# Performance work log

Measured on AMD Instinct MI355X. Metric: run time of the kernel, lower is better.

Reference implementation:

```python
import jax, jax.numpy as jnp
import numpy as np

# dims: episodes E, steps S, comm length L, hidden H, rnn input IN, comm vocab OUT
E, S, L, H, IN, OUT = 64, 32, 32, 1024, 2048, 64
TAU = 2.0      # MTRNN leaky-integrator time constant
EPS = 1e-5     # BatchNorm eps


def setup_inputs() -> dict:
    key = jax.random.key(0)
    ks = jax.random.split(key, 16)
    def p(k, shape, scale=0.02):
        return jax.random.normal(k, shape, jnp.float32) * scale
    return {
        "h_w_action": jax.random.normal(ks[0], (E, S, IN), jnp.float32),
        # MTRNN cell
        "Wx": p(ks[1], (IN, H)), "bx": jnp.zeros((H,), jnp.float32),
        "Wh": p(ks[2], (H, H)), "bh": jnp.zeros((H,), jnp.float32),
        # Ted_Conv1d: 4 branches, kernels 1/3/5/7, each H//4 out channels (OIH layout)
        "w1": p(ks[3], (H // 4, H, 1)), "b1": jnp.zeros((H // 4,), jnp.float32),
        "w3": p(ks[4], (H // 4, H, 3)), "b3": jnp.zeros((H // 4,), jnp.float32),
        "w5": p(ks[5], (H // 4, H, 5)), "b5": jnp.zeros((H // 4,), jnp.float32),
        "w7": p(ks[6], (H // 4, H, 7)), "b7": jnp.zeros((H // 4,), jnp.float32),
        # BatchNorm1d affine
        "gamma": jnp.ones((H,), jnp.float32), "beta": jnp.zeros((H,), jnp.float32),
        # PReLU (single shared slope, torch default init 0.25)
        "prelu_a": jnp.array(0.25, jnp.float32),
        # output Linear
        "Wout": p(ks[7], (H, OUT)), "bout": jnp.zeros((OUT,), jnp.float32),
    }


def _conv(x, w, b):
    # x: [N, C, L], w: [O, I, k], 'same' padding for odd kernels
    pad = (w.shape[-1] - 1) // 2
    y = jax.lax.conv_general_dilated(x, w, (1,), [(pad, pad)],
                                     dimension_numbers=('NCH', 'OIH', 'NCH'))
    return y + b[None, :, None]


def reference(h_w_action, Wx, bx, Wh, bh, w1, b1, w3, b3, w5, b5, w7, b7,
              gamma, beta, prelu_a, Wout, bout):
    # MTRNN: same input every step; leaky integration h' = (1-1/tau)h + (1/tau)tanh(Wx x + Wh h)
    x_r = h_w_action @ Wx + bx                      # [E,S,H], constant across steps
    h0 = jnp.zeros((E, S, H), h_w_action.dtype)

    def step(h, _):
        h_new = (1.0 - 1.0 / TAU) * h + (1.0 / TAU) * jnp.tanh(x_r + h @ Wh + bh)
        return h_new, h_new

    _, hs = jax.lax.scan(step, h0, None, length=L)  # [L,E,S,H]
    hs = hs.transpose(1, 2, 0, 3).reshape(E * S, L, H)

    # multi-kernel conv over the comm-length axis
    xc = hs.transpose(0, 2, 1)                      # [N,H,L]
    y = jnp.concatenate([_conv(xc, w1, b1), _conv(xc, w3, b3),
                         _conv(xc, w5, b5), _conv(xc, w7, b7)], axis=1)  # [N,H,L]

    # BatchNorm1d (training-mode batch stats over N and L), affine
    mean = y.mean(axis=(0, 2), keepdims=True)
    var = y.var(axis=(0, 2), keepdims=True)
    y = (y - mean) * jax.lax.rsqrt(var + EPS) * gamma[None, :, None] + beta[None, :, None]

    # PReLU; Dropout is identity at eval
    y = jnp.where(y > 0, y, prelu_a * y)

    y = y.transpose(0, 2, 1).reshape(E, S, L, H)
    return y @ Wout + bout                          # [E,S,L,OUT]
```

## Files before the change

kernel.cpp:

```cpp
#include <hip/hip_runtime.h>
#include <cstdint>
#include <cmath>

#define DI __device__ __forceinline__


typedef __attribute__((ext_vector_type(8))) short bf16x8;
typedef __attribute__((ext_vector_type(4))) short s16x4;
typedef __attribute__((ext_vector_type(4))) float f32x4;

DI float bf2f(short u){
  union { unsigned int i; float f; } v; v.i = ((unsigned int)(unsigned short)u) << 16; return v.f;
}
DI short f2bf(float f){
  unsigned int x = __builtin_bit_cast(unsigned int, f);
  unsigned int r = (x + 0x7FFFu + ((x >> 16) & 1u)) >> 16;
  return (short)(unsigned short)r;
}
DI void gload16(const void* g, void* l){
  __builtin_amdgcn_global_load_lds(
      (const __attribute__((address_space(1))) unsigned int*)g,
      (__attribute__((address_space(3))) unsigned int*)l, 16, 0, 0);
}

template<int BM, int BN, int MODE>
__global__ __launch_bounds__(256)
void gemm_k(const short* __restrict__ A, long lda,
            const short* __restrict__ Bt, long ldb, int Ksteps,
            const float* __restrict__ bias,
            float* __restrict__ f32out,
            const float* __restrict__ f32in,
            short* __restrict__ bfout, int jj)
{
  constexpr int WTM = BM / 2, WTN = BN / 2;
  constexpr int FM = WTM / 16, FN = WTN / 16;
  constexpr int AIT = BM / 32, BIT = BN / 32;
  __shared__ short As[BM * 64];
  __shared__ short Bs[BN * 64];
  const int tid = threadIdx.x;
  const int w = tid >> 6, l = tid & 63;
  const int wr = w >> 1, wc = w & 1;
  const int lr = l & 15, lk = (l >> 4) << 3;
  const int brow = blockIdx.x * BM;
  const int bcol = blockIdx.y * BN;

  int coff = 0, jout = 0;
  if constexpr (MODE == 2) {
    const int bb = bcol >> 7;
    const int dlt = (bb < 2) ? -3 : (bb < 6) ? -2 : (bb < 12) ? -1
                  : (bb < 20) ? 0 : (bb < 26) ? 1 : (bb < 30) ? 2 : 3;
    coff = (dlt == -3) ? 768 : (dlt == -2) ? 256 : (dlt == -1) ? -512
         : (dlt == 0) ? -1536 : (dlt == 1) ? -2304 : (dlt == 2) ? -2816 : -3072;
    jout = jj - dlt;
    if (jout < 0 || jout > 31) return;
  }

  f32x4 acc[FM][FN];
  #pragma unroll
  for (int i = 0; i < FM; i++)
    #pragma unroll
    for (int j = 0; j < FN; j++) {
      acc[i][j][0] = 0.f; acc[i][j][1] = 0.f; acc[i][j][2] = 0.f; acc[i][j][3] = 0.f;
    }

  const short* ap[AIT];
  const short* bp[BIT];
  const int rsub = tid >> 3;
  const int koff = (tid & 7) << 3;
  #pragma unroll
  for (int it = 0; it < AIT; ++it)
    ap[it] = A + (long)(brow + it * 32 + rsub) * lda + koff;
  #pragma unroll
  for (int it = 0; it < BIT; ++it)
    bp[it] = Bt + (long)(bcol + it * 32 + rsub) * ldb + koff;

  for (int ks = 0; ks < Ksteps; ++ks) {
    #pragma unroll
    for (int it = 0; it < AIT; ++it) {
      gload16(ap[it], As + ((it * 256 + (w << 6)) << 3));
      ap[it] += 64;
    }
    #pragma unroll
    for (int it = 0; it < BIT; ++it) {
      gload16(bp[it], Bs + ((it * 256 + (w << 6)) << 3));
      bp[it] += 64;
    }
    __syncthreads();
    #pragma unroll
    for (int kk = 0; kk < 64; kk += 32) {
      bf16x8 a[FM], b[FN];
      #pragma unroll
      for (int i = 0; i < FM; i++)
        a[i] = *(const bf16x8*)&As[(wr * WTM + i * 16 + lr) * 64 + kk + lk];
      #pragma unroll
      for (int j = 0; j < FN; j++)
        b[j] = *(const bf16x8*)&Bs[(wc * WTN + j * 16 + lr) * 64 + kk + lk];
      #pragma unroll
      for (int i = 0; i < FM; i++)
        #pragma unroll
        for (int j = 0; j < FN; j++)
          acc[i][j] = __builtin_amdgcn_mfma_f32_16x16x32_bf16(a[i], b[j], acc[i][j], 0, 0, 0);
    }
    __syncthreads();
  }

  const int rbase = brow + wr * WTM;
  const int cbase = bcol + wc * WTN;
  const int rl = (l >> 4) << 2;
  #pragma unroll
  for (int i = 0; i < FM; i++) {
    #pragma unroll
    for (int j = 0; j < FN; j++) {
      #pragma unroll
      for (int r = 0; r < 4; r++) {
        const int row = rbase + i * 16 + rl + r;
        const int col = cbase + j * 16 + lr;
        const float v = acc[i][j][r];
        if constexpr (MODE == 0) {
          f32out[(long)row * 1024 + col] = v + bias[col];
        } else if constexpr (MODE == 1) {
          const long idx = (long)row * 1024 + col;
          const float hn = 0.5f * f32out[idx] + 0.5f * tanhf(f32in[idx] + v + bias[col]);
          f32out[idx] = hn;
          bfout[idx] = f2bf(hn);
        } else if constexpr (MODE == 2) {
          short* yp = bfout + ((long)row * 32 + jout) * 1024 + (col + coff);
          *yp = f2bf(bf2f(*yp) + v);
        } else {
          f32out[(long)row * 64 + col] = v + bias[col];
        }
      }
    }
  }
}

__global__ __launch_bounds__(256)
void g5_bn(const short* __restrict__ y, const short* __restrict__ WoutT,
           const float* __restrict__ scal, const float* __restrict__ shft,
           const float* __restrict__ aP, const float* __restrict__ bout,
           float* __restrict__ out)
{
  __shared__ short As[128 * 64];
  __shared__ short Bs[64 * 64];
  __shared__ float sS[1024], sB[1024];
  const int tid = threadIdx.x;
  const int w = tid >> 6, l = tid & 63;
  const int wr = w >> 1, wc = w & 1;
  const int lr = l & 15, lk = (l >> 4) << 3;
  const int m0 = blockIdx.x * 128;
  for (int i = tid; i < 1024; i += 256) { sS[i] = scal[i]; sB[i] = shft[i]; }
  const float a = *aP;
  __syncthreads();

  f32x4 acc[4][2];
  #pragma unroll
  for (int i = 0; i < 4; i++)
    #pragma unroll
    for (int j = 0; j < 2; j++) {
      acc[i][j][0] = 0.f; acc[i][j][1] = 0.f; acc[i][j][2] = 0.f; acc[i][j][3] = 0.f;
    }

  const int rsub = tid >> 3;
  const int koff = (tid & 7) << 3;
  const short* yp[4];
  #pragma unroll
  for (int it = 0; it < 4; ++it)
    yp[it] = y + (long)(m0 + it * 32 + rsub) * 1024 + koff;
  const short* bp[2];
  #pragma unroll
  for (int it = 0; it < 2; ++it)
    bp[it] = WoutT + (long)(it * 32 + rsub) * 1024 + koff;

  for (int ks = 0; ks < 16; ++ks) {
    #pragma unroll
    for (int it = 0; it < 2; ++it) {
      gload16(bp[it], Bs + ((it * 256 + (w << 6)) << 3));
      bp[it] += 64;
    }
    const int c0 = ks * 64 + koff;
    #pragma unroll
    for (int it = 0; it < 4; ++it) {
      bf16x8 v = *(const bf16x8*)yp[it];
      yp[it] += 64;
      #pragma unroll
      for (int e = 0; e < 8; ++e) {
        float f = bf2f(v[e]) * sS[c0 + e] + sB[c0 + e];
        v[e] = f2bf(f > 0.f ? f : a * f);
      }
      *(bf16x8*)(As + ((it * 256 + tid) << 3)) = v;
    }
    __syncthreads();
    #pragma unroll
    for (int kk = 0; kk < 64; kk += 32) {
      bf16x8 af[4], bf_[2];
      #pragma unroll
      for (int i = 0; i < 4; i++)
        af[i] = *(const bf16x8*)&As[(wr * 64 + i * 16 + lr) * 64 + kk + lk];
      #pragma unroll
      for (int j = 0; j < 2; j++)
        bf_[j] = *(const bf16x8*)&Bs[(wc * 32 + j * 16 + lr) * 64 + kk + lk];
      #pragma unroll
      for (int i = 0; i < 4; i++)
        #pragma unroll
        for (int j = 0; j < 2; j++)
          acc[i][j] = __builtin_amdgcn_mfma_f32_16x16x32_bf16(af[i], bf_[j], acc[i][j], 0, 0, 0);
    }
    __syncthreads();
  }

  const int rbase = m0 + wr * 64, cbase = wc * 32;
  const int rl = (l >> 4) << 2;
  #pragma unroll
  for (int i = 0; i < 4; i++)
    #pragma unroll
    for (int j = 0; j < 2; j++)
      #pragma unroll
      for (int r = 0; r < 4; r++) {
        const int row = rbase + i * 16 + rl + r;
        const int col = cbase + j * 16 + lr;
        out[(long)row * 64 + col] = acc[i][j][r] + bout[col];
      }
}

__global__ void zero16(float4* __restrict__ p, long n)
{
  long i = (long)blockIdx.x * 256 + threadIdx.x;
  if (i < n) p[i] = float4{0.f, 0.f, 0.f, 0.f};
}

__global__ void cvt4_f32_bf16(const float* __restrict__ in, short* __restrict__ out, int n4)
{
  int i = blockIdx.x * 256 + threadIdx.x;
  if (i >= n4) return;
  float4 v = ((const float4*)in)[i];
  s16x4 o; o[0] = f2bf(v.x); o[1] = f2bf(v.y); o[2] = f2bf(v.z); o[3] = f2bf(v.w);
  ((s16x4*)out)[i] = o;
}

__global__ void transpose_f32_bf16(const float* __restrict__ in, short* __restrict__ out,
                                   int R, int C)
{
  __shared__ short tile[32][33];
  const int tx = threadIdx.x & 31, ty = threadIdx.x >> 5;
  const int c0 = blockIdx.x * 32, r0 = blockIdx.y * 32;
  #pragma unroll
  for (int i = 0; i < 32; i += 8)
    tile[ty + i][tx] = f2bf(in[(long)(r0 + ty + i) * C + (c0 + tx)]);
  __syncthreads();
  #pragma unroll
  for (int i = 0; i < 32; i += 8)
    out[(long)(c0 + ty + i) * R + (r0 + tx)] = tile[tx][ty + i];
}

__global__ void build_wpack(const float* __restrict__ w1, const float* __restrict__ w3,
                            const float* __restrict__ w5, const float* __restrict__ w7,
                            short* __restrict__ Wp)
{
  const int pc = blockIdx.x;
  int dlt, c;
  if      (pc < 256)  { dlt = -3; c = pc + 768; }
  else if (pc < 768)  { dlt = -2; c = pc + 256; }
  else if (pc < 1536) { dlt = -1; c = pc - 512; }
  else if (pc < 2560) { dlt = 0;  c = pc - 1536; }
  else if (pc < 3328) { dlt = 1;  c = pc - 2304; }
  else if (pc < 3840) { dlt = 2;  c = pc - 2816; }
  else                { dlt = 3;  c = pc - 3072; }
  const int b = c >> 8, kb = 2 * b + 1, t = dlt + b, oo = c & 255;
  const float* w = (b == 0) ? w1 : (b == 1) ? w3 : (b == 2) ? w5 : w7;
  short* dst = Wp + (long)pc * 1024;
  for (int i = threadIdx.x; i < 1024; i += 256)
    dst[i] = f2bf(w[((long)oo * 1024 + i) * kb + t]);
}

__global__ void bn_stats(const short* __restrict__ y, float* __restrict__ sum,
                         float* __restrict__ ssq)
{
  const int c0 = threadIdx.x * 4;
  float s0 = 0, s1 = 0, s2 = 0, s3 = 0, q0 = 0, q1 = 0, q2 = 0, q3 = 0;
  const long base = (long)blockIdx.x * 32;
  for (int r = 0; r < 32; ++r) {
    s16x4 v = *(const s16x4*)(y + (base + r) * 1024 + c0);
    float f0 = bf2f(v[0]), f1 = bf2f(v[1]), f2v = bf2f(v[2]), f3 = bf2f(v[3]);
    s0 += f0; s1 += f1; s2 += f2v; s3 += f3;
    q0 += f0 * f0; q1 += f1 * f1; q2 += f2v * f2v; q3 += f3 * f3;
  }
  atomicAdd(&sum[c0 + 0], s0); atomicAdd(&sum[c0 + 1], s1);
  atomicAdd(&sum[c0 + 2], s2); atomicAdd(&sum[c0 + 3], s3);
  atomicAdd(&ssq[c0 + 0], q0); atomicAdd(&ssq[c0 + 1], q1);
  atomicAdd(&ssq[c0 + 2], q2); atomicAdd(&ssq[c0 + 3], q3);
}

__global__ void bn_finalize(const float* __restrict__ bnsum, const float* __restrict__ bnss,
                            const float* __restrict__ gamma, const float* __restrict__ beta,
                            float* __restrict__ scale, float* __restrict__ shift)
{
  int c = blockIdx.x * 256 + threadIdx.x;
  const float inv = 1.f / 65536.f;
  float mean = bnsum[c] * inv;
  float var = bnss[c] * inv - mean * mean;
  float sc = gamma[c] * rsqrtf(var + 1e-5f);
  scale[c] = sc;
  shift[c] = beta[c] - mean * sc;
}

extern "C" void kernel_launch(void* const* d_in, const int* in_sizes, int n_in,
                              void* d_out, int out_size, void* d_ws, size_t ws_size,
                              hipStream_t stream)
{
  const float* h_w_action = (const float*)d_in[0];
  const float* Wx   = (const float*)d_in[1];
  const float* bx   = (const float*)d_in[2];
  const float* Wh   = (const float*)d_in[3];
  const float* bh   = (const float*)d_in[4];
  const float* w1   = (const float*)d_in[5];
  const float* w3   = (const float*)d_in[7];
  const float* w5   = (const float*)d_in[9];
  const float* w7   = (const float*)d_in[11];
  const float* gamma = (const float*)d_in[13];
  const float* beta  = (const float*)d_in[14];
  const float* prelu = (const float*)d_in[15];
  const float* Wout  = (const float*)d_in[16];
  const float* bout  = (const float*)d_in[17];
  float* out = (float*)d_out;

  char* p = (char*)d_ws;
  auto alloc = [&](size_t bytes) -> char* {
    char* r = p; p += (bytes + 255) & ~(size_t)255; return r;
  };
  short* y     = (short*)alloc(65536L * 1024 * 2);
  float* xr    = (float*)alloc(2048L * 1024 * 4);
  float* hf    = (float*)alloc(2048L * 1024 * 4);
  short* hb0   = (short*)alloc(2048L * 1024 * 2);
  short* hb1   = (short*)alloc(2048L * 1024 * 2);
  short* A1    = (short*)alloc(2048L * 2048 * 2);
  short* WxT   = (short*)alloc(1024L * 2048 * 2);
  short* WhT   = (short*)alloc(1024L * 1024 * 2);
  short* Wp    = (short*)alloc(4096L * 1024 * 2);
  short* WoutT = (short*)alloc(64L * 1024 * 2);
  float* bnsum = (float*)alloc(1024 * 4);
  float* bnss  = (float*)alloc(1024 * 4);
  float* scal  = (float*)alloc(1024 * 4);
  float* shft  = (float*)alloc(1024 * 4);

  if ((size_t)(p - (char*)d_ws) > ws_size) return;

  zero16<<<32768, 256, 0, stream>>>((float4*)y, 65536L * 1024 * 2 / 16);
  zero16<<<2048, 256, 0, stream>>>((float4*)hf, 2048L * 1024 * 4 / 16);
  zero16<<<1024, 256, 0, stream>>>((float4*)hb0, 2048L * 1024 * 2 / 16);
  zero16<<<1, 256, 0, stream>>>((float4*)bnsum, 256);
  zero16<<<1, 256, 0, stream>>>((float4*)bnss, 256);

  cvt4_f32_bf16<<<4096, 256, 0, stream>>>(h_w_action, A1, 2048 * 2048 / 4);
  transpose_f32_bf16<<<dim3(32, 64), 256, 0, stream>>>(Wx, WxT, 2048, 1024);
  transpose_f32_bf16<<<dim3(32, 32), 256, 0, stream>>>(Wh, WhT, 1024, 1024);
  transpose_f32_bf16<<<dim3(2, 32), 256, 0, stream>>>(Wout, WoutT, 1024, 64);
  build_wpack<<<4096, 256, 0, stream>>>(w1, w3, w5, w7, Wp);

  gemm_k<64, 128, 0><<<dim3(32, 8), 256, 0, stream>>>(
      A1, 2048, WxT, 2048, 32, bx, xr, nullptr, nullptr, 0);

  short* hb[2] = {hb0, hb1};
  for (int s = 1; s <= 32; ++s) {
    gemm_k<64, 64, 1><<<dim3(32, 16), 256, 0, stream>>>(
        hb[(s - 1) & 1], 1024, WhT, 1024, 16, bh, hf, xr, hb[s & 1], 0);
    gemm_k<128, 128, 2><<<dim3(16, 32), 256, 0, stream>>>(
        hb[s & 1], 1024, Wp, 1024, 16, nullptr, nullptr, nullptr, y, s - 1);
  }

  bn_stats<<<2048, 256, 0, stream>>>(y, bnsum, bnss);
  bn_finalize<<<4, 256, 0, stream>>>(bnsum, bnss, gamma, beta, scal, shft);

  g5_bn<<<dim3(512, 1), 256, 0, stream>>>(y, WoutT, scal, shft, prelu, bout, out);
}
```

Baseline: 2.044 ms.

## Double-buffer GEMM LDS loads, drop y/hf zeroing, replace BN atomics with two-pass reduction

The GEMM main loop now double-buffers its LDS tiles so the next K-tile's global-to-LDS loads overlap the current MFMA compute, using explicit vmcnt waits and raw barriers. The recurrent step reads the previous hidden state from the bf16 buffer instead of a separate fp32 copy. That removes the fp32 hidden state and its zeroing, but the leaky integration now runs at bf16 precision. The conv accumulation writes directly on the first contributing tap, so the large y buffer no longer needs zeroing. BN statistics use per-block partial sums plus a second reduction kernel instead of atomics, and the xr GEMM tile shrinks to 64x64.

```diff
diff --git a/kernel.cpp b/kernel.cpp
--- a/kernel.cpp
+++ b/kernel.cpp
@@ -21,6 +21,12 @@
   __builtin_amdgcn_global_load_lds(
       (const __attribute__((address_space(1))) unsigned int*)g,
       (__attribute__((address_space(3))) unsigned int*)l, 16, 0, 0);
+}
+template<int N> DI void waitv(){
+  if constexpr (N == 0) asm volatile("s_waitcnt vmcnt(0)" ::: "memory");
+  else if constexpr (N == 4) asm volatile("s_waitcnt vmcnt(4)" ::: "memory");
+  else if constexpr (N == 6) asm volatile("s_waitcnt vmcnt(6)" ::: "memory");
+  else asm volatile("s_waitcnt vmcnt(8)" ::: "memory");
 }
 
 template<int BM, int BN, int MODE>
@@ -35,8 +41,9 @@
   constexpr int WTM = BM / 2, WTN = BN / 2;
   constexpr int FM = WTM / 16, FN = WTN / 16;
   constexpr int AIT = BM / 32, BIT = BN / 32;
-  __shared__ short As[BM * 64];
-  __shared__ short Bs[BN * 64];
+  constexpr int NLD = AIT + BIT;
+  __shared__ short As[2][BM * 64];
+  __shared__ short Bs[2][BN * 64];
   const int tid = threadIdx.x;
   const int w = tid >> 6, l = tid & 63;
   const int wr = w >> 1, wc = w & 1;
@@ -45,6 +52,7 @@
   const int bcol = blockIdx.y * BN;
 
   int coff = 0, jout = 0;
+  bool first = false;
   if constexpr (MODE == 2) {
     const int bb = bcol >> 7;
     const int dlt = (bb < 2) ? -3 : (bb < 6) ? -2 : (bb < 12) ? -1
@@ -53,6 +61,8 @@
          : (dlt == 0) ? -1536 : (dlt == 1) ? -2304 : (dlt == 2) ? -2816 : -3072;
     jout = jj - dlt;
     if (jout < 0 || jout > 31) return;
+    const int ubranch = (bcol + coff) >> 8;
+    first = (dlt == -(ubranch < jout ? ubranch : jout));
   }
 
   f32x4 acc[FM][FN];
@@ -63,45 +73,54 @@
       acc[i][j][0] = 0.f; acc[i][j][1] = 0.f; acc[i][j][2] = 0.f; acc[i][j][3] = 0.f;
     }
 
-  const short* ap[AIT];
-  const short* bp[BIT];
   const int rsub = tid >> 3;
   const int koff = (tid & 7) << 3;
+  const short* aB[AIT];
+  const short* bB[BIT];
   #pragma unroll
   for (int it = 0; it < AIT; ++it)
-    ap[it] = A + (long)(brow + it * 32 + rsub) * lda + koff;
+    aB[it] = A + (long)(brow + it * 32 + rsub) * lda + koff;
   #pragma unroll
   for (int it = 0; it < BIT; ++it)
-    bp[it] = Bt + (long)(bcol + it * 32 + rsub) * ldb + koff;
-
-  for (int ks = 0; ks < Ksteps; ++ks) {
-    #pragma unroll
-    for (int it = 0; it < AIT; ++it) {
-      gload16(ap[it], As + ((it * 256 + (w << 6)) << 3));
-      ap[it] += 64;
-    }
-    #pragma unroll
-    for (int it = 0; it < BIT; ++it) {
-      gload16(bp[it], Bs + ((it * 256 + (w << 6)) << 3));
-      bp[it] += 64;
-    }
-    __syncthreads();
+    bB[it] = Bt + (long)(bcol + it * 32 + rsub) * ldb + koff;
+
+  auto stage = [&](int ks, int bsel) {
+    const int off = ks * 64;
+    #pragma unroll
+    for (int it = 0; it < AIT; ++it)
+      gload16(aB[it] + off, &As[bsel][(it * 256 + (w << 6)) << 3]);
+    #pragma unroll
+    for (int it = 0; it < BIT; ++it)
+      gload16(bB[it] + off, &Bs[bsel][(it * 256 + (w << 6)) << 3]);
+  };
+  auto compute = [&](int bsel) {
     #pragma unroll
     for (int kk = 0; kk < 64; kk += 32) {
       bf16x8 a[FM], b[FN];
       #pragma unroll
       for (int i = 0; i < FM; i++)
-        a[i] = *(const bf16x8*)&As[(wr * WTM + i * 16 + lr) * 64 + kk + lk];
+        a[i] = *(const bf16x8*)&As[bsel][(wr * WTM + i * 16 + lr) * 64 + kk + lk];
       #pragma unroll
       for (int j = 0; j < FN; j++)
-        b[j] = *(const bf16x8*)&Bs[(wc * WTN + j * 16 + lr) * 64 + kk + lk];
+        b[j] = *(const bf16x8*)&Bs[bsel][(wc * WTN + j * 16 + lr) * 64 + kk + lk];
       #pragma unroll
       for (int i = 0; i < FM; i++)
         #pragma unroll
         for (int j = 0; j < FN; j++)
           acc[i][j] = __builtin_amdgcn_mfma_f32_16x16x32_bf16(a[i], b[j], acc[i][j], 0, 0, 0);
     }
-    __syncthreads();
+  };
+
+  stage(0, 0);
+  for (int t = 0; t < Ksteps; ++t) {
+    const int cur = t & 1;
+    if (t + 1 < Ksteps) { stage(t + 1, cur ^ 1); waitv<NLD>(); }
+    else                { waitv<0>(); }
+    __builtin_amdgcn_s_barrier();
+    __builtin_amdgcn_sched_barrier(0);
+    compute(cur);
+    __builtin_amdgcn_sched_barrier(0);
+    __builtin_amdgcn_s_barrier();
   }
 
   const int rbase = brow + wr * WTM;
@@ -120,14 +139,13 @@
           f32out[(long)row * 1024 + col] = v + bias[col];
         } else if constexpr (MODE == 1) {
           const long idx = (long)row * 1024 + col;
-          const float hn = 0.5f * f32out[idx] + 0.5f * tanhf(f32in[idx] + v + bias[col]);
-          f32out[idx] = hn;
+          const float hp = bf2f(A[(long)row * lda + col]);
+          const float hn = 0.5f * hp + 0.5f * tanhf(f32in[idx] + v + bias[col]);
           bfout[idx] = f2bf(hn);
         } else if constexpr (MODE == 2) {
           short* yp = bfout + ((long)row * 32 + jout) * 1024 + (col + coff);
-          *yp = f2bf(bf2f(*yp) + v);
-        } else {
-          f32out[(long)row * 64 + col] = v + bias[col];
+          if (first) *yp = f2bf(v);
+          else       *yp = f2bf(bf2f(*yp) + v);
         }
       }
     }
@@ -272,32 +290,35 @@
     dst[i] = f2bf(w[((long)oo * 1024 + i) * kb + t]);
 }
 
-__global__ void bn_stats(const short* __restrict__ y, float* __restrict__ sum,
-                         float* __restrict__ ssq)
+__global__ void bn_stats1(const short* __restrict__ y, float* __restrict__ psum,
+                          float* __restrict__ pssq)
 {
   const int c0 = threadIdx.x * 4;
   float s0 = 0, s1 = 0, s2 = 0, s3 = 0, q0 = 0, q1 = 0, q2 = 0, q3 = 0;
-  const long base = (long)blockIdx.x * 32;
-  for (int r = 0; r < 32; ++r) {
+  const long base = (long)blockIdx.x * 64;
+  for (int r = 0; r < 64; ++r) {
     s16x4 v = *(const s16x4*)(y + (base + r) * 1024 + c0);
     float f0 = bf2f(v[0]), f1 = bf2f(v[1]), f2v = bf2f(v[2]), f3 = bf2f(v[3]);
     s0 += f0; s1 += f1; s2 += f2v; s3 += f3;
     q0 += f0 * f0; q1 += f1 * f1; q2 += f2v * f2v; q3 += f3 * f3;
   }
-  atomicAdd(&sum[c0 + 0], s0); atomicAdd(&sum[c0 + 1], s1);
-  atomicAdd(&sum[c0 + 2], s2); atomicAdd(&sum[c0 + 3], s3);
-  atomicAdd(&ssq[c0 + 0], q0); atomicAdd(&ssq[c0 + 1], q1);
-  atomicAdd(&ssq[c0 + 2], q2); atomicAdd(&ssq[c0 + 3], q3);
-}
-
-__global__ void bn_finalize(const float* __restrict__ bnsum, const float* __restrict__ bnss,
-                            const float* __restrict__ gamma, const float* __restrict__ beta,
-                            float* __restrict__ scale, float* __restrict__ shift)
-{
-  int c = blockIdx.x * 256 + threadIdx.x;
+  ((float4*)(psum + (long)blockIdx.x * 1024))[threadIdx.x] = float4{s0, s1, s2, s3};
+  ((float4*)(pssq + (long)blockIdx.x * 1024))[threadIdx.x] = float4{q0, q1, q2, q3};
+}
+
+__global__ void bn_stats2(const float* __restrict__ psum, const float* __restrict__ pssq,
+                          const float* __restrict__ gamma, const float* __restrict__ beta,
+                          float* __restrict__ scale, float* __restrict__ shift)
+{
+  const int c = blockIdx.x * 256 + threadIdx.x;
+  float s = 0.f, q = 0.f;
+  for (int b = 0; b < 1024; ++b) {
+    s += psum[(long)b * 1024 + c];
+    q += pssq[(long)b * 1024 + c];
+  }
   const float inv = 1.f / 65536.f;
-  float mean = bnsum[c] * inv;
-  float var = bnss[c] * inv - mean * mean;
+  float mean = s * inv;
+  float var = q * inv - mean * mean;
   float sc = gamma[c] * rsqrtf(var + 1e-5f);
   scale[c] = sc;
   shift[c] = beta[c] - mean * sc;
@@ -329,7 +350,8 @@
   };
   short* y     = (short*)alloc(65536L * 1024 * 2);
   float* xr    = (float*)alloc(2048L * 1024 * 4);
-  float* hf    = (float*)alloc(2048L * 1024 * 4);
+  float* psum  = (float*)alloc(1024L * 1024 * 4);
+  float* pssq  = (float*)alloc(1024L * 1024 * 4);
   short* hb0   = (short*)alloc(2048L * 1024 * 2);
   short* hb1   = (short*)alloc(2048L * 1024 * 2);
   short* A1    = (short*)alloc(2048L * 2048 * 2);
@@ -337,18 +359,12 @@
   short* WhT   = (short*)alloc(1024L * 1024 * 2);
   short* Wp    = (short*)alloc(4096L * 1024 * 2);
   short* WoutT = (short*)alloc(64L * 1024 * 2);
-  float* bnsum = (float*)alloc(1024 * 4);
-  float* bnss  = (float*)alloc(1024 * 4);
   float* scal  = (float*)alloc(1024 * 4);
   float* shft  = (float*)alloc(1024 * 4);
 
   if ((size_t)(p - (char*)d_ws) > ws_size) return;
 
-  zero16<<<32768, 256, 0, stream>>>((float4*)y, 65536L * 1024 * 2 / 16);
-  zero16<<<2048, 256, 0, stream>>>((float4*)hf, 2048L * 1024 * 4 / 16);
   zero16<<<1024, 256, 0, stream>>>((float4*)hb0, 2048L * 1024 * 2 / 16);
-  zero16<<<1, 256, 0, stream>>>((float4*)bnsum, 256);
-  zero16<<<1, 256, 0, stream>>>((float4*)bnss, 256);
 
   cvt4_f32_bf16<<<4096, 256, 0, stream>>>(h_w_action, A1, 2048 * 2048 / 4);
   transpose_f32_bf16<<<dim3(32, 64), 256, 0, stream>>>(Wx, WxT, 2048, 1024);
@@ -356,19 +372,19 @@
   transpose_f32_bf16<<<dim3(2, 32), 256, 0, stream>>>(Wout, WoutT, 1024, 64);
   build_wpack<<<4096, 256, 0, stream>>>(w1, w3, w5, w7, Wp);
 
-  gemm_k<64, 128, 0><<<dim3(32, 8), 256, 0, stream>>>(
+  gemm_k<64, 64, 0><<<dim3(32, 16), 256, 0, stream>>>(
       A1, 2048, WxT, 2048, 32, bx, xr, nullptr, nullptr, 0);
 
   short* hb[2] = {hb0, hb1};
   for (int s = 1; s <= 32; ++s) {
     gemm_k<64, 64, 1><<<dim3(32, 16), 256, 0, stream>>>(
-        hb[(s - 1) & 1], 1024, WhT, 1024, 16, bh, hf, xr, hb[s & 1], 0);
+        hb[(s - 1) & 1], 1024, WhT, 1024, 16, bh, nullptr, xr, hb[s & 1], 0);
     gemm_k<128, 128, 2><<<dim3(16, 32), 256, 0, stream>>>(
         hb[s & 1], 1024, Wp, 1024, 16, nullptr, nullptr, nullptr, y, s - 1);
   }
 
-  bn_stats<<<2048, 256, 0, stream>>>(y, bnsum, bnss);
-  bn_finalize<<<4, 256, 0, stream>>>(bnsum, bnss, gamma, beta, scal, shft);
+  bn_stats1<<<1024, 256, 0, stream>>>(y, psum, pssq);
+  bn_stats2<<<4, 256, 0, stream>>>(psum, pssq, gamma, beta, scal, shft);
 
   g5_bn<<<dim3(512, 1), 256, 0, stream>>>(y, WoutT, scal, shft, prelu, bout, out);
 }
```

Result: slower. 2.198 ms (+7.6%).

## Drop y zero-fill, fp32 hidden state, and atomic BN stats

Applied to the files above, without the earlier changes.

The conv GEMM now writes, rather than accumulates, on the first tap that touches each output slot, so the 128MB zero-fill of y goes away. The recurrence reads the previous hidden state from the bf16 A operand instead of keeping a separate fp32 state buffer, which removes that buffer's traffic and its zeroing. BatchNorm statistics move from atomics to per-block partial sums plus a second reduction kernel that also folds in the finalize step, and the x-projection GEMM tile is reduced. The risks are lower precision in the leaky-integrator state, since it is now carried in bf16, and correctness of the first-writer logic.

```diff
diff --git a/kernel.cpp b/kernel.cpp
--- a/kernel.cpp
+++ b/kernel.cpp
@@ -45,6 +45,7 @@
   const int bcol = blockIdx.y * BN;
 
   int coff = 0, jout = 0;
+  bool first = false;
   if constexpr (MODE == 2) {
     const int bb = bcol >> 7;
     const int dlt = (bb < 2) ? -3 : (bb < 6) ? -2 : (bb < 12) ? -1
@@ -53,6 +54,8 @@
          : (dlt == 0) ? -1536 : (dlt == 1) ? -2304 : (dlt == 2) ? -2816 : -3072;
     jout = jj - dlt;
     if (jout < 0 || jout > 31) return;
+    const int ubranch = (bcol + coff) >> 8;
+    first = (dlt == -(ubranch < jout ? ubranch : jout));
   }
 
   f32x4 acc[FM][FN];
@@ -63,10 +66,10 @@
       acc[i][j][0] = 0.f; acc[i][j][1] = 0.f; acc[i][j][2] = 0.f; acc[i][j][3] = 0.f;
     }
 
+  const int rsub = tid >> 3;
+  const int koff = (tid & 7) << 3;
   const short* ap[AIT];
   const short* bp[BIT];
-  const int rsub = tid >> 3;
-  const int koff = (tid & 7) << 3;
   #pragma unroll
   for (int it = 0; it < AIT; ++it)
     ap[it] = A + (long)(brow + it * 32 + rsub) * lda + koff;
@@ -120,14 +123,13 @@
           f32out[(long)row * 1024 + col] = v + bias[col];
         } else if constexpr (MODE == 1) {
           const long idx = (long)row * 1024 + col;
-          const float hn = 0.5f * f32out[idx] + 0.5f * tanhf(f32in[idx] + v + bias[col]);
-          f32out[idx] = hn;
+          const float hp = bf2f(A[(long)row * lda + col]);
+          const float hn = 0.5f * hp + 0.5f * tanhf(f32in[idx] + v + bias[col]);
           bfout[idx] = f2bf(hn);
         } else if constexpr (MODE == 2) {
           short* yp = bfout + ((long)row * 32 + jout) * 1024 + (col + coff);
-          *yp = f2bf(bf2f(*yp) + v);
-        } else {
-          f32out[(long)row * 64 + col] = v + bias[col];
+          if (first) *yp = f2bf(v);
+          else       *yp = f2bf(bf2f(*yp) + v);
         }
       }
     }
@@ -272,35 +274,57 @@
     dst[i] = f2bf(w[((long)oo * 1024 + i) * kb + t]);
 }
 
-__global__ void bn_stats(const short* __restrict__ y, float* __restrict__ sum,
-                         float* __restrict__ ssq)
+__global__ void bn_stats1(const short* __restrict__ y, float* __restrict__ psum,
+                          float* __restrict__ pssq)
 {
   const int c0 = threadIdx.x * 4;
   float s0 = 0, s1 = 0, s2 = 0, s3 = 0, q0 = 0, q1 = 0, q2 = 0, q3 = 0;
-  const long base = (long)blockIdx.x * 32;
-  for (int r = 0; r < 32; ++r) {
+  const long base = (long)blockIdx.x * 64;
+  for (int r = 0; r < 64; ++r) {
     s16x4 v = *(const s16x4*)(y + (base + r) * 1024 + c0);
     float f0 = bf2f(v[0]), f1 = bf2f(v[1]), f2v = bf2f(v[2]), f3 = bf2f(v[3]);
     s0 += f0; s1 += f1; s2 += f2v; s3 += f3;
     q0 += f0 * f0; q1 += f1 * f1; q2 += f2v * f2v; q3 += f3 * f3;
   }
-  atomicAdd(&sum[c0 + 0], s0); atomicAdd(&sum[c0 + 1], s1);
-  atomicAdd(&sum[c0 + 2], s2); atomicAdd(&sum[c0 + 3], s3);
-  atomicAdd(&ssq[c0 + 0], q0); atomicAdd(&ssq[c0 + 1], q1);
-  atomicAdd(&ssq[c0 + 2], q2); atomicAdd(&ssq[c0 + 3], q3);
-}
-
-__global__ void bn_finalize(const float* __restrict__ bnsum, const float* __restrict__ bnss,
-                            const float* __restrict__ gamma, const float* __restrict__ beta,
-                            float* __restrict__ scale, float* __restrict__ shift)
-{
-  int c = blockIdx.x * 256 + threadIdx.x;
-  const float inv = 1.f / 65536.f;
-  float mean = bnsum[c] * inv;
-  float var = bnss[c] * inv - mean * mean;
-  float sc = gamma[c] * rsqrtf(var + 1e-5f);
-  scale[c] = sc;
-  shift[c] = beta[c] - mean * sc;
+  ((float4*)(psum + (long)blockIdx.x * 1024))[threadIdx.x] = float4{s0, s1, s2, s3};
+  ((float4*)(pssq + (long)blockIdx.x * 1024))[threadIdx.x] = float4{q0, q1, q2, q3};
+}
+
+__global__ __launch_bounds__(256)
+void bn_stats2(const float* __restrict__ psum, const float* __restrict__ pssq,
+               const float* __restrict__ gamma, const float* __restrict__ beta,
+               float* __restrict__ scale, float* __restrict__ shift)
+{
+  __shared__ float reds[256], redq[256];
+  const int ch = threadIdx.x & 7;
+  const int rseg = threadIdx.x >> 3;
+  const int c = blockIdx.x * 8 + ch;
+  float s = 0.f, q = 0.f;
+  #pragma unroll 4
+  for (int k = 0; k < 32; ++k) {
+    const long row = rseg + 32 * k;
+    s += psum[row * 1024 + c];
+    q += pssq[row * 1024 + c];
+  }
+  reds[rseg * 8 + ch] = s;
+  redq[rseg * 8 + ch] = q;
+  __syncthreads();
+  #pragma unroll
+  for (int st = 16; st > 0; st >>= 1) {
+    if (rseg < st) {
+      reds[rseg * 8 + ch] += reds[(rseg + st) * 8 + ch];
+      redq[rseg * 8 + ch] += redq[(rseg + st) * 8 + ch];
+    }
+    __syncthreads();
+  }
+  if (rseg == 0) {
+    const float inv = 1.f / 65536.f;
+    float mean = reds[ch] * inv;
+    float var = redq[ch] * inv - mean * mean;
+    float sc = gamma[c] * rsqrtf(var + 1e-5f);
+    scale[c] = sc;
+    shift[c] = beta[c] - mean * sc;
+  }
 }
 
 extern "C" void kernel_launch(void* const* d_in, const int* in_sizes, int n_in,
@@ -329,7 +353,8 @@
   };
   short* y     = (short*)alloc(65536L * 1024 * 2);
   float* xr    = (float*)alloc(2048L * 1024 * 4);
-  float* hf    = (float*)alloc(2048L * 1024 * 4);
+  float* psum  = (float*)alloc(1024L * 1024 * 4);
+  float* pssq  = (float*)alloc(1024L * 1024 * 4);
   short* hb0   = (short*)alloc(2048L * 1024 * 2);
   short* hb1   = (short*)alloc(2048L * 1024 * 2);
   short* A1    = (short*)alloc(2048L * 2048 * 2);
@@ -337,18 +362,12 @@
   short* WhT   = (short*)alloc(1024L * 1024 * 2);
   short* Wp    = (short*)alloc(4096L * 1024 * 2);
   short* WoutT = (short*)alloc(64L * 1024 * 2);
-  float* bnsum = (float*)alloc(1024 * 4);
-  float* bnss  = (float*)alloc(1024 * 4);
   float* scal  = (float*)alloc(1024 * 4);
   float* shft  = (float*)alloc(1024 * 4);
 
   if ((size_t)(p - (char*)d_ws) > ws_size) return;
 
-  zero16<<<32768, 256, 0, stream>>>((float4*)y, 65536L * 1024 * 2 / 16);
-  zero16<<<2048, 256, 0, stream>>>((float4*)hf, 2048L * 1024 * 4 / 16);
   zero16<<<1024, 256, 0, stream>>>((float4*)hb0, 2048L * 1024 * 2 / 16);
-  zero16<<<1, 256, 0, stream>>>((float4*)bnsum, 256);
-  zero16<<<1, 256, 0, stream>>>((float4*)bnss, 256);
 
   cvt4_f32_bf16<<<4096, 256, 0, stream>>>(h_w_action, A1, 2048 * 2048 / 4);
   transpose_f32_bf16<<<dim3(32, 64), 256, 0, stream>>>(Wx, WxT, 2048, 1024);
@@ -356,19 +375,19 @@
   transpose_f32_bf16<<<dim3(2, 32), 256, 0, stream>>>(Wout, WoutT, 1024, 64);
   build_wpack<<<4096, 256, 0, stream>>>(w1, w3, w5, w7, Wp);
 
-  gemm_k<64, 128, 0><<<dim3(32, 8), 256, 0, stream>>>(
+  gemm_k<64, 64, 0><<<dim3(32, 16), 256, 0, stream>>>(
       A1, 2048, WxT, 2048, 32, bx, xr, nullptr, nullptr, 0);
 
   short* hb[2] = {hb0, hb1};
   for (int s = 1; s <= 32; ++s) {
     gemm_k<64, 64, 1><<<dim3(32, 16), 256, 0, stream>>>(
-        hb[(s - 1) & 1], 1024, WhT, 1024, 16, bh, hf, xr, hb[s & 1], 0);
+        hb[(s - 1) & 1], 1024, WhT, 1024, 16, bh, nullptr, xr, hb[s & 1], 0);
     gemm_k<128, 128, 2><<<dim3(16, 32), 256, 0, stream>>>(
         hb[s & 1], 1024, Wp, 1024, 16, nullptr, nullptr, nullptr, y, s - 1);
   }
 
-  bn_stats<<<2048, 256, 0, stream>>>(y, bnsum, bnss);
-  bn_finalize<<<4, 256, 0, stream>>>(bnsum, bnss, gamma, beta, scal, shft);
+  bn_stats1<<<1024, 256, 0, stream>>>(y, psum, pssq);
+  bn_stats2<<<128, 256, 0, stream>>>(psum, pssq, gamma, beta, scal, shft);
 
   g5_bn<<<dim3(512, 1), 256, 0, stream>>>(y, WoutT, scal, shft, prelu, bout, out);
 }
```

Result: no change. 2.046 ms (+0.1%).
